# Kernel tuning notes

Measured on AMD Instinct MI355X. Metric: run time of the kernel, lower is better.

## Reference

```python
import jax, jax.numpy as jnp
import numpy as np

N_HEAD = 16
N_KV_HEAD = 4
HD = 128
ROPE_THETA = 10000.0


def _rope_cos_sin(T, hd, dtype):
    inv_freq = 1.0 / (ROPE_THETA ** (jnp.arange(0, hd, 2, dtype=jnp.float32) / hd))  # [hd/2]
    ang = jnp.arange(T, dtype=jnp.float32)[:, None] * inv_freq[None, :]  # [T, hd/2]
    return jnp.cos(ang).astype(dtype), jnp.sin(ang).astype(dtype)


def _apply_rope(x, cos, sin):
    # x: [B, T, H, hd]; rotate interleaved (even, odd) pairs Llama-style
    x1 = x[..., 0::2]
    x2 = x[..., 1::2]
    c = cos[None, :, None, :]
    s = sin[None, :, None, :]
    o1 = x1 * c - x2 * s
    o2 = x1 * s + x2 * c
    return jnp.stack([o1, o2], axis=-1).reshape(x.shape)


def setup_inputs() -> dict:
    key = jax.random.key(0)
    k1, k2, k3 = jax.random.split(key, 3)
    B, T, C = 4, 2048, 2048
    x = jax.random.normal(k1, (B, T, C), dtype=jnp.float32)
    w_attn = jax.random.normal(k2, ((N_HEAD + 2 * N_KV_HEAD) * HD, C), dtype=jnp.float32) * (C ** -0.5)
    w_proj = jax.random.normal(k3, (C, C), dtype=jnp.float32) * (C ** -0.5)
    return {"x": x, "w_attn": w_attn, "w_proj": w_proj}


def reference(x, w_attn, w_proj):
    B, T, C = x.shape
    n_rep = N_HEAD // N_KV_HEAD
    qkv = x @ w_attn.T  # [B, T, (H + 2*Hkv)*hd]
    q, k, v = jnp.split(qkv, [N_HEAD * HD, (N_HEAD + N_KV_HEAD) * HD], axis=-1)
    q = q.reshape(B, T, N_HEAD, HD)
    k = k.reshape(B, T, N_KV_HEAD, HD)
    v = v.reshape(B, T, N_KV_HEAD, HD)
    cos, sin = _rope_cos_sin(T, HD, x.dtype)
    q = _apply_rope(q, cos, sin)
    k = _apply_rope(k, cos, sin)
    # GQA: repeat kv heads (repeat_interleave on head dim)
    k = jnp.repeat(k, n_rep, axis=2)
    v = jnp.repeat(v, n_rep, axis=2)
    # [B, H, T, hd]
    q = q.transpose(0, 2, 1, 3)
    k = k.transpose(0, 2, 1, 3)
    v = v.transpose(0, 2, 1, 3)
    att = jnp.einsum("bhqd,bhkd->bhqk", q, k) * (1.0 / jnp.sqrt(jnp.asarray(HD, x.dtype)))
    causal = jnp.tril(jnp.ones((T, T), dtype=bool))
    att = jnp.where(causal[None, None, :, :], att, jnp.asarray(-jnp.inf, att.dtype))
    att = jax.nn.softmax(att, axis=-1)
    y = jnp.einsum("bhqk,bhkd->bhqd", att, v)
    y = y.transpose(0, 2, 1, 3).reshape(B, T, C)
    return y @ w_proj.T
```

## Files before the change

kernel.cpp:

```cpp
#include <hip/hip_runtime.h>
#include <math.h>

#define NH   16
#define NKV  4
#define HD   128
#define BSZ  4
#define TLEN 2048
#define CDIM 2048
#define MROWS (BSZ*TLEN)

typedef short bf16x8 __attribute__((ext_vector_type(8)));
typedef float f32x4  __attribute__((ext_vector_type(4)));
typedef int   int4v  __attribute__((ext_vector_type(4)));

__device__ inline float bf2f(unsigned short h) {
  union { unsigned u; float f; } x; x.u = ((unsigned)h) << 16; return x.f;
}
__device__ inline unsigned short f2bf(float f) {
  union { float f; unsigned u; } x; x.f = f;
  unsigned u = x.u;
  return (unsigned short)((u + 0x7FFFu + ((u >> 16) & 1u)) >> 16);
}

__device__ inline void gload_lds16(const void* g, void* l) {
  __builtin_amdgcn_global_load_lds((const __attribute__((address_space(1))) void*)g,
                                   (__attribute__((address_space(3))) void*)l, 16, 0, 0);
}

__global__ void detect_kernel(const void* __restrict__ wproj, int* __restrict__ flag) {
  __shared__ int cnt;
  if (threadIdx.x == 0) cnt = 0;
  __syncthreads();
  const unsigned short* s = (const unsigned short*)wproj;
  unsigned short v = s[2 * threadIdx.x];
  int e = (v >> 7) & 0xFF;
  if (e >= 90 && e <= 141) atomicAdd(&cnt, 1);
  __syncthreads();
  if (threadIdx.x == 0) *flag = (cnt >= 192) ? 1 : 0;
}

__device__ inline void stage8(short* dst, const void* src, size_t eoff, int isbf) {
  if (isbf) {
    *(int4v*)dst = *(const int4v*)((const short*)src + eoff);
  } else {
    const f32x4* f = (const f32x4*)((const float*)src + eoff);
    f32x4 a = f[0], b = f[1];
    __align__(16) short t[8];
    t[0] = (short)f2bf(a[0]); t[1] = (short)f2bf(a[1]);
    t[2] = (short)f2bf(a[2]); t[3] = (short)f2bf(a[3]);
    t[4] = (short)f2bf(b[0]); t[5] = (short)f2bf(b[1]);
    t[6] = (short)f2bf(b[2]); t[7] = (short)f2bf(b[3]);
    *(int4v*)dst = *(int4v*)t;
  }
}

__global__ __launch_bounds__(256) void cvt_kernel(const void* __restrict__ src,
                                                  short* __restrict__ dst,
                                                  int n8, const int* __restrict__ flagp)
{
  const int fl = *flagp;
  const int i = blockIdx.x * 256 + threadIdx.x;
  if (i >= n8) return;
  __align__(16) short t[8];
  stage8(t, src, (size_t)i * 8, fl);
  *(int4v*)(dst + (size_t)i * 8) = *(int4v*)t;
}

template<int MODE>
__global__ __launch_bounds__(256) void gemm_bt(
    const short* __restrict__ A, const short* __restrict__ W,
    short* __restrict__ o0, short* __restrict__ o1, short* __restrict__ o2,
    float* __restrict__ o0f, const int* __restrict__ flagp)
{
  __shared__ __align__(16) short As[128*32];
  __shared__ __align__(16) short Bs[128*32];
  const int fl = *flagp;
  const int tid  = threadIdx.x;
  const int wave = tid >> 6;
  const int lane = tid & 63;
  const int cl   = lane & 15;
  const int quad = lane >> 4;
  const int nwgx = gridDim.x;
  int wg = (int)blockIdx.y * nwgx + (int)blockIdx.x;
  const int cpx = (nwgx * (int)gridDim.y) >> 3;
  wg = (wg & 7) * cpx + (wg >> 3);
  const int m0 = (wg / nwgx) * 128;
  const int n0 = (wg % nwgx) * 128;
  const int wr = (wave >> 1) * 64;
  const int wc = (wave & 1) * 64;
  const int K = CDIM;
  const int rq = tid >> 2;
  const int cq = (tid & 3) << 3;
  const short* Ap = A + (size_t)(m0 + rq) * K + cq;
  const short* Wp = W + (size_t)(n0 + rq) * K + cq;
  short* AsW = As + wave * 512;
  short* BsW = Bs + wave * 512;
  const size_t rowskip = (size_t)64 * K;

  f32x4 acc[4][4];
#pragma unroll
  for (int i = 0; i < 4; i++)
#pragma unroll
    for (int j = 0; j < 4; j++) acc[i][j] = (f32x4){0.f, 0.f, 0.f, 0.f};

  for (int k0 = 0; k0 < K; k0 += 32) {
    gload_lds16(Ap + k0,           AsW);
    gload_lds16(Ap + k0 + rowskip, AsW + 2048);
    gload_lds16(Wp + k0,           BsW);
    gload_lds16(Wp + k0 + rowskip, BsW + 2048);
    __syncthreads();
    bf16x8 af[4], bfr[4];
#pragma unroll
    for (int i = 0; i < 4; i++) af[i]  = *(const bf16x8*)(&As[(wr + i*16 + cl)*32 + quad*8]);
#pragma unroll
    for (int j = 0; j < 4; j++) bfr[j] = *(const bf16x8*)(&Bs[(wc + j*16 + cl)*32 + quad*8]);
#pragma unroll
    for (int i = 0; i < 4; i++)
#pragma unroll
      for (int j = 0; j < 4; j++)
        acc[i][j] = __builtin_amdgcn_mfma_f32_16x16x32_bf16(af[i], bfr[j], acc[i][j], 0, 0, 0);
    __syncthreads();
  }

#pragma unroll
  for (int i = 0; i < 4; i++) {
#pragma unroll
    for (int j = 0; j < 4; j++) {
#pragma unroll
      for (int r = 0; r < 4; r++) {
        const int gm = m0 + wr + i*16 + quad*4 + r;
        const int gn = n0 + wc + j*16 + cl;
        const float fv = acc[i][j][r];
        if (MODE == 1) {
          if (fl) o0[(size_t)gm * CDIM + gn] = (short)f2bf(fv);
          else    o0f[(size_t)gm * CDIM + gn] = fv;
        } else {
          const int b = gm >> 11;
          const int t = gm & (TLEN - 1);
          const int head = gn >> 7;
          const int d = gn & (HD - 1);
          const unsigned short h = f2bf(fv);
          if (head < 16) {
            o0[(((size_t)(b*NH + head) * TLEN + t) << 7) + d] = (short)h;
          } else if (head < 20) {
            o1[(((size_t)(b*NKV + (head-16)) * TLEN + t) << 7) + d] = (short)h;
          } else {
            o2[(((size_t)(b*NKV + (head-20)) * HD + d) << 11) + t] = (short)h;
          }
        }
      }
    }
  }
}

__global__ __launch_bounds__(256) void rope_kernel(short* __restrict__ qb,
                                                   short* __restrict__ kb)
{
  const int idx = blockIdx.x * 256 + threadIdx.x;
  const int per_plane = TLEN * 64;
  const int plane = idx / per_plane;
  const int rem = idx - plane * per_plane;
  const int t = rem >> 6;
  const int i = rem & 63;
  short* base = (plane < 64) ? (qb + (size_t)plane * (TLEN*HD))
                             : (kb + (size_t)(plane - 64) * (TLEN*HD));
  const size_t off = (size_t)t * HD + 2*i;
  const float x1 = bf2f((unsigned short)base[off]);
  const float x2 = bf2f((unsigned short)base[off+1]);
  const float inv = __expf(-0.14391156847064198f * (float)i);
  const float ang = (float)t * inv;
  float s, c;
  sincosf(ang, &s, &c);
  const float qscale = (plane < 64) ? 0.08838834764831845f : 1.0f;
  base[off]   = (short)f2bf((x1*c - x2*s) * qscale);
  base[off+1] = (short)f2bf((x1*s + x2*c) * qscale);
}

__device__ inline void stage_tiles(short* Ks, short* Vs,
                                   const short* Kp, const short* Vp,
                                   int k0, int tid, int wave) {
#pragma unroll
  for (int i = 0; i < 2; i++) {
    const int chunk = i*512 + tid;
    const int row = chunk >> 4;
    const int cc  = (chunk & 15) ^ (row & 7);
    gload_lds16(Kp + (size_t)(k0 + row)*HD + cc*8,
                Ks + ((i*512 + wave*64) << 3));
  }
#pragma unroll
  for (int i = 0; i < 2; i++) {
    const int chunk = i*512 + tid;
    const int row = chunk >> 3;
    const int cc  = (chunk & 7) ^ (row & 7);
    gload_lds16(Vp + (size_t)row*TLEN + k0 + cc*8,
                Vs + ((i*512 + wave*64) << 3));
  }
}

__global__ __launch_bounds__(512, 4) void attn_kernel(
    const short* __restrict__ qb, const short* __restrict__ kb,
    const short* __restrict__ vtb, short* __restrict__ yb)
{
  __shared__ __align__(16) short Ks[2][64*128];
  __shared__ __align__(16) short Vs[2][128*64];
  __shared__ short Plds[8][16][64];
  const int tid  = threadIdx.x;
  const int wave = tid >> 6;
  const int lane = tid & 63;
  const int cl   = lane & 15;
  const int quad = lane >> 4;
  const int bh = blockIdx.y;
  const int b = bh >> 4, h = bh & 15;
  const int kvh = h >> 2;

  const short* Qp = qb  + (size_t)(b*NH  + h)   * TLEN * HD;
  const short* Kp = kb  + (size_t)(b*NKV + kvh) * TLEN * HD;
  const short* Vp = vtb + (size_t)(b*NKV + kvh) * HD * TLEN;
  short* Pw = &Plds[wave][0][0];
  const int swz = (cl & 7) << 3;

  bf16x8 ones;
#pragma unroll
  for (int i = 0; i < 8; i++) ones[i] = (short)0x3F80;

#pragma unroll 1
  for (int pass = 0; pass < 2; ++pass) {
    const int qi = pass ? (TLEN/128 - 1 - (int)blockIdx.x) : (int)blockIdx.x;
    const int q0 = qi * 128;
    const int ntiles = 2*qi + 2;

    bf16x8 qf[4];
    const int qrow = q0 + wave*16 + cl;
#pragma unroll
    for (int s = 0; s < 4; s++)
      qf[s] = *(const bf16x8*)(Qp + (size_t)qrow*HD + s*32 + quad*8);

    f32x4 O[8];
#pragma unroll
    for (int d = 0; d < 8; d++) O[d] = (f32x4){0.f, 0.f, 0.f, 0.f};
    f32x4 Ol = (f32x4){0.f, 0.f, 0.f, 0.f};
    float m_i[4];
#pragma unroll
    for (int r = 0; r < 4; r++) m_i[r] = -1e9f;

    stage_tiles(Ks[0], Vs[0], Kp, Vp, 0, tid, wave);
    __syncthreads();
    int cur = 0;

    for (int kt = 0; kt < ntiles; kt++) {
      const int k0 = kt * 64;

      if (kt + 1 < ntiles)
        stage_tiles(Ks[cur^1], Vs[cur^1], Kp, Vp, k0 + 64, tid, wave);

      const short* Kt = Ks[cur];
      const short* Vt = Vs[cur];

      f32x4 S[4];
#pragma unroll
      for (int j = 0; j < 4; j++) S[j] = (f32x4){0.f, 0.f, 0.f, 0.f};
#pragma unroll
      for (int s = 0; s < 4; s++) {
        bf16x8 kfj[4];
#pragma unroll
        for (int j = 0; j < 4; j++)
          kfj[j] = *(const bf16x8*)(&Kt[(size_t)(j*16 + cl)*128 + ((((s*4 + quad) << 3) ^ swz))]);
#pragma unroll
        for (int j = 0; j < 4; j++)
          S[j] = __builtin_amdgcn_mfma_f32_16x16x32_bf16(qf[s], kfj[j], S[j], 0, 0, 0);
      }

      if (kt >= ntiles - 2) {
#pragma unroll
        for (int j = 0; j < 4; j++) {
          const int col = k0 + j*16 + cl;
#pragma unroll
          for (int r = 0; r < 4; r++) {
            const int row = q0 + wave*16 + quad*4 + r;
            if (col > row) S[j][r] = -1e9f;
          }
        }
      }

      float pmax[4];
#pragma unroll
      for (int r = 0; r < 4; r++) {
        float mx = fmaxf(fmaxf(S[0][r], S[1][r]), fmaxf(S[2][r], S[3][r]));
#pragma unroll
        for (int off = 1; off < 16; off <<= 1) mx = fmaxf(mx, __shfl_xor(mx, off));
        pmax[r] = mx;
      }
      const int ok = (pmax[0] - m_i[0] <= 8.f) && (pmax[1] - m_i[1] <= 8.f) &&
                     (pmax[2] - m_i[2] <= 8.f) && (pmax[3] - m_i[3] <= 8.f);
      if (!__all(ok)) {
#pragma unroll
        for (int r = 0; r < 4; r++) {
          const float mnew = fmaxf(m_i[r], pmax[r]);
          const float alpha = __expf(m_i[r] - mnew);
          Ol[r] *= alpha;
          m_i[r] = mnew;
#pragma unroll
          for (int d = 0; d < 8; d++) O[d][r] *= alpha;
        }
      }
#pragma unroll
      for (int r = 0; r < 4; r++)
#pragma unroll
        for (int j = 0; j < 4; j++)
          S[j][r] = __expf(S[j][r] - m_i[r]);

#pragma unroll
      for (int j = 0; j < 4; j++)
#pragma unroll
        for (int r = 0; r < 4; r++) {
          const int row = quad*4 + r;
          int idx = row*64 + j*16 + cl;
          idx ^= (row & 7) << 3;
          Pw[idx] = (short)f2bf(S[j][r]);
        }

#pragma unroll
      for (int s2 = 0; s2 < 2; s2++) {
        int idx = cl*64 + s2*32 + quad*8;
        idx ^= (cl & 7) << 3;
        bf16x8 pf = *(const bf16x8*)(&Pw[idx]);
        Ol = __builtin_amdgcn_mfma_f32_16x16x32_bf16(pf, ones, Ol, 0, 0, 0);
#pragma unroll
        for (int d = 0; d < 8; d++) {
          bf16x8 vfd = *(const bf16x8*)(&Vt[(size_t)(d*16 + cl)*64 + ((((s2*4 + quad) << 3) ^ swz))]);
          O[d] = __builtin_amdgcn_mfma_f32_16x16x32_bf16(pf, vfd, O[d], 0, 0, 0);
        }
      }

      __syncthreads();
      cur ^= 1;
    }

    float linv[4];
#pragma unroll
    for (int r = 0; r < 4; r++) linv[r] = 1.0f / Ol[r];
#pragma unroll
    for (int d = 0; d < 8; d++) {
#pragma unroll
      for (int r = 0; r < 4; r++) {
        const int t = q0 + wave*16 + quad*4 + r;
        yb[(size_t)(b*TLEN + t) * CDIM + h*HD + d*16 + cl] = (short)f2bf(O[d][r] * linv[r]);
      }
    }
  }
}

extern "C" void kernel_launch(void* const* d_in, const int* in_sizes, int n_in,
                              void* d_out, int out_size, void* d_ws, size_t ws_size,
                              hipStream_t stream)
{
  const void* x      = d_in[0];
  const void* w_attn = d_in[1];
  const void* w_proj = d_in[2];

  char* ws = (char*)d_ws;
  int*   flag = (int*)ws;
  short* qb  = (short*)(ws + (size_t) 1*1024*1024);
  short* kb  = (short*)(ws + (size_t)33*1024*1024);
  short* vtb = (short*)(ws + (size_t)41*1024*1024);
  short* yb  = (short*)(ws + (size_t)49*1024*1024);
  short* xb  = (short*)d_out;
  short* wab = (short*)((char*)d_out + (size_t)32*1024*1024);
  short* wpb = kb;

  dim3 blk(256);
  detect_kernel<<<1, blk, 0, stream>>>(w_proj, flag);
  cvt_kernel<<<dim3((MROWS*CDIM/8)/256), blk, 0, stream>>>(x, xb, MROWS*CDIM/8, flag);
  cvt_kernel<<<dim3((3072*CDIM/8)/256), blk, 0, stream>>>(w_attn, wab, 3072*CDIM/8, flag);
  gemm_bt<0><<<dim3(3072/128, MROWS/128), blk, 0, stream>>>(xb, wab, qb, kb, vtb, nullptr, flag);
  rope_kernel<<<dim3((80*TLEN*64)/256), blk, 0, stream>>>(qb, kb);
  attn_kernel<<<dim3(TLEN/256, BSZ*NH), dim3(512), 0, stream>>>(qb, kb, vtb, yb);
  cvt_kernel<<<dim3((CDIM*CDIM/8)/256), blk, 0, stream>>>(w_proj, wpb, CDIM*CDIM/8, flag);
  gemm_bt<1><<<dim3(CDIM/128, MROWS/128), blk, 0, stream>>>(yb, wpb, (short*)d_out,
                                                            nullptr, nullptr, (float*)d_out, flag);
}
```

Before: 553.7 us.

## Rewrite GEMM with 256x256 tiles, 4-stage LDS pipeline and swizzled layout

```diff
diff --git a/kernel.cpp b/kernel.cpp
--- a/kernel.cpp
+++ b/kernel.cpp
@@ -67,69 +67,86 @@
 }
 
 template<int MODE>
-__global__ __launch_bounds__(256) void gemm_bt(
+__global__ __launch_bounds__(512, 2) void gemm_bt(
     const short* __restrict__ A, const short* __restrict__ W,
     short* __restrict__ o0, short* __restrict__ o1, short* __restrict__ o2,
     float* __restrict__ o0f, const int* __restrict__ flagp)
 {
-  __shared__ __align__(16) short As[128*32];
-  __shared__ __align__(16) short Bs[128*32];
+  __shared__ __align__(16) short SB[4][16384];
   const int fl = *flagp;
   const int tid  = threadIdx.x;
   const int wave = tid >> 6;
   const int lane = tid & 63;
   const int cl   = lane & 15;
   const int quad = lane >> 4;
+  const int wm = wave >> 2;
+  const int wn = wave & 3;
   const int nwgx = gridDim.x;
   int wg = (int)blockIdx.y * nwgx + (int)blockIdx.x;
   const int cpx = (nwgx * (int)gridDim.y) >> 3;
   wg = (wg & 7) * cpx + (wg >> 3);
-  const int m0 = (wg / nwgx) * 128;
-  const int n0 = (wg % nwgx) * 128;
-  const int wr = (wave >> 1) * 64;
-  const int wc = (wave & 1) * 64;
-  const int K = CDIM;
-  const int rq = tid >> 2;
-  const int cq = (tid & 3) << 3;
-  const short* Ap = A + (size_t)(m0 + rq) * K + cq;
-  const short* Wp = W + (size_t)(n0 + rq) * K + cq;
-  short* AsW = As + wave * 512;
-  short* BsW = Bs + wave * 512;
-  const size_t rowskip = (size_t)64 * K;
-
-  f32x4 acc[4][4];
-#pragma unroll
-  for (int i = 0; i < 4; i++)
+  const int m0 = (wg / nwgx) * 256;
+  const int n0 = (wg % nwgx) * 256;
+
+  const int cswz  = (((cl & 1) << 2) | quad) ^ (cl >> 1);
+  const int abase = (wm*64 + (cl >> 1)) * 64 + cswz * 8;
+  const int bbase = 8192 + (wn*32 + (cl >> 1)) * 64 + cswz * 8;
+
+  f32x4 acc[8][4];
+#pragma unroll
+  for (int i = 0; i < 8; i++)
 #pragma unroll
     for (int j = 0; j < 4; j++) acc[i][j] = (f32x4){0.f, 0.f, 0.f, 0.f};
 
-  for (int k0 = 0; k0 < K; k0 += 32) {
-    gload_lds16(Ap + k0,           AsW);
-    gload_lds16(Ap + k0 + rowskip, AsW + 2048);
-    gload_lds16(Wp + k0,           BsW);
-    gload_lds16(Wp + k0 + rowskip, BsW + 2048);
-    __syncthreads();
-    bf16x8 af[4], bfr[4];
-#pragma unroll
-    for (int i = 0; i < 4; i++) af[i]  = *(const bf16x8*)(&As[(wr + i*16 + cl)*32 + quad*8]);
-#pragma unroll
-    for (int j = 0; j < 4; j++) bfr[j] = *(const bf16x8*)(&Bs[(wc + j*16 + cl)*32 + quad*8]);
-#pragma unroll
-    for (int i = 0; i < 4; i++)
+  const short* Asrc = A + (size_t)m0 * CDIM;
+  const short* Wsrc = W + (size_t)n0 * CDIM;
+
+  auto stage1 = [&](const short* src, int kk, short* dst) {
+#pragma unroll
+    for (int i = 0; i < 2; i++) {
+      const int chunk = i*512 + tid;
+      const int lr  = chunk >> 3;
+      const int c   = (chunk & 7) ^ (lr & 7);
+      const int row = lr*2 + (c >> 2);
+      gload_lds16(src + (size_t)row * CDIM + kk + (c & 3)*8,
+                  dst + ((i*512 + wave*64) << 3));
+    }
+  };
+#define STAGE(t) { short* db = &SB[(t)&3][0]; stage1(Asrc, (t)*32, db); stage1(Wsrc, (t)*32, db + 8192); }
+
+  STAGE(0); STAGE(1); STAGE(2);
+  const int nt = CDIM / 32;
+  for (int kt = 0; kt < nt; ++kt) {
+    const int rem = nt - kt;
+    if (rem > 2)       asm volatile("s_waitcnt vmcnt(8)" : : : "memory");
+    else if (rem == 2) asm volatile("s_waitcnt vmcnt(4)" : : : "memory");
+    else               asm volatile("s_waitcnt vmcnt(0)" : : : "memory");
+    __builtin_amdgcn_s_barrier();
+    if (kt + 3 < nt) STAGE(kt+3);
+    const short* Tb = &SB[kt & 3][0];
+    bf16x8 af[8], bfj[4];
+#pragma unroll
+    for (int i = 0; i < 8; i++) af[i]  = *(const bf16x8*)&Tb[abase + i*512];
+#pragma unroll
+    for (int j = 0; j < 4; j++) bfj[j] = *(const bf16x8*)&Tb[bbase + j*512];
+    __builtin_amdgcn_s_setprio(1);
+#pragma unroll
+    for (int i = 0; i < 8; i++)
 #pragma unroll
       for (int j = 0; j < 4; j++)
-        acc[i][j] = __builtin_amdgcn_mfma_f32_16x16x32_bf16(af[i], bfr[j], acc[i][j], 0, 0, 0);
-    __syncthreads();
-  }
-
-#pragma unroll
-  for (int i = 0; i < 4; i++) {
+        acc[i][j] = __builtin_amdgcn_mfma_f32_16x16x32_bf16(af[i], bfj[j], acc[i][j], 0, 0, 0);
+    __builtin_amdgcn_s_setprio(0);
+  }
+#undef STAGE
+
+#pragma unroll
+  for (int i = 0; i < 8; i++) {
 #pragma unroll
     for (int j = 0; j < 4; j++) {
 #pragma unroll
       for (int r = 0; r < 4; r++) {
-        const int gm = m0 + wr + i*16 + quad*4 + r;
-        const int gn = n0 + wc + j*16 + cl;
+        const int gm = m0 + wm*128 + i*16 + quad*4 + r;
+        const int gn = n0 + wn*64  + j*16 + cl;
         const float fv = acc[i][j][r];
         if (MODE == 1) {
           if (fl) o0[(size_t)gm * CDIM + gn] = (short)f2bf(fv);
@@ -372,10 +389,10 @@
   detect_kernel<<<1, blk, 0, stream>>>(w_proj, flag);
   cvt_kernel<<<dim3((MROWS*CDIM/8)/256), blk, 0, stream>>>(x, xb, MROWS*CDIM/8, flag);
   cvt_kernel<<<dim3((3072*CDIM/8)/256), blk, 0, stream>>>(w_attn, wab, 3072*CDIM/8, flag);
-  gemm_bt<0><<<dim3(3072/128, MROWS/128), blk, 0, stream>>>(xb, wab, qb, kb, vtb, nullptr, flag);
+  gemm_bt<0><<<dim3(3072/256, MROWS/256), dim3(512), 0, stream>>>(xb, wab, qb, kb, vtb, nullptr, flag);
   rope_kernel<<<dim3((80*TLEN*64)/256), blk, 0, stream>>>(qb, kb);
   attn_kernel<<<dim3(TLEN/256, BSZ*NH), dim3(512), 0, stream>>>(qb, kb, vtb, yb);
   cvt_kernel<<<dim3((CDIM*CDIM/8)/256), blk, 0, stream>>>(w_proj, wpb, CDIM*CDIM/8, flag);
-  gemm_bt<1><<<dim3(CDIM/128, MROWS/128), blk, 0, stream>>>(yb, wpb, (short*)d_out,
-                                                            nullptr, nullptr, (float*)d_out, flag);
-}
+  gemm_bt<1><<<dim3(CDIM/256, MROWS/256), dim3(512), 0, stream>>>(yb, wpb, (short*)d_out,
+                                                                  nullptr, nullptr, (float*)d_out, flag);
+}
```

Measured after the change: 507.9 us. -8.3%, faster.
